# Performance work log

Hardware: AMD Instinct MI355X
Metric: run time of the kernel (lower is better)

Reference implementation:

```python
import jax, jax.numpy as jnp
import numpy as np

EPS = 1e-4
MAX_LAPLACE_VAR = 1000.0
MAX_DENSITY = 10000.0
BINS = 256

_LAP_KERNEL = jnp.array([[0., 1., 0.], [1., -4., 1.], [0., 1., 0.]], dtype=jnp.float32)[None, None]  # OIHW [1,1,3,3]


def setup_inputs() -> dict:
    key = jax.random.key(0)
    k1, k2 = jax.random.split(key)
    rgb_img = jax.random.uniform(k1, (32, 3, 512, 512), dtype=jnp.float32)
    depth_img = jax.random.normal(k2, (32, 1, 512, 512), dtype=jnp.float32)
    return {"rgb_img": rgb_img, "depth_img": depth_img}


def _rgb_confidence(rgb_img):
    B, C, H, W = rgb_img.shape
    gray = 0.299 * rgb_img[:, 0] + 0.587 * rgb_img[:, 1] + 0.114 * rgb_img[:, 2]  # [B,H,W]
    gray = gray[:, None]  # [B,1,H,W]
    lap = jax.lax.conv_general_dilated(
        gray, _LAP_KERNEL, window_strides=(1, 1), padding=[(1, 1), (1, 1)],
        dimension_numbers=("NCHW", "OIHW", "NCHW"))
    # torch.var default is unbiased (ddof=1)
    laplace_var = jnp.var(lap, axis=(1, 2, 3), ddof=1)

    # integer-valued pixels 0..255 land exactly in histc bins 0..255 (bins=256, min=0, max=255)
    vals = jnp.clip(gray * 255.0, 0.0, 255.0).astype(jnp.int32)  # [B,1,H,W]
    vals = vals.reshape(B, -1)  # [B, H*W]
    bidx = jnp.broadcast_to(jnp.arange(B)[:, None], vals.shape)
    hist = jnp.zeros((B, BINS), jnp.float32).at[bidx, vals].add(1.0)
    p = hist / jnp.sum(hist, axis=1, keepdims=True)
    entropy = -jnp.sum(p * jnp.log2(p + EPS), axis=1)

    clarity_score = laplace_var / (MAX_LAPLACE_VAR + EPS)
    uniformity_score = 1.0 / (entropy + EPS)
    return (0.5 * (clarity_score + uniformity_score))[:, None]  # [B,1]


def _depth_confidence(depth_img):
    C = depth_img.shape[1]
    depth_map = depth_img[:, 2] if C == 3 else depth_img[:, 0]  # [B,H,W]
    mask = (depth_map > 0).astype(jnp.float32)
    density = jnp.mean(mask, axis=(1, 2))

    # vectorized masked std (unbiased, ddof=1), matching torch.std over valid pixels
    n = jnp.sum(mask, axis=(1, 2))  # [B]
    mean = jnp.sum(depth_map * mask, axis=(1, 2)) / jnp.maximum(n, 1.0)
    sq = jnp.sum(mask * (depth_map - mean[:, None, None]) ** 2, axis=(1, 2))
    var = sq / jnp.maximum(n - 1.0, 1.0)
    std = jnp.sqrt(jnp.maximum(var, 0.0))
    noise_level = jnp.where(n > 0, std, 1.0)

    density_score = density / (MAX_DENSITY + EPS)
    noise_score = 1.0 / (noise_level + EPS)
    return (0.5 * (density_score + noise_score))[:, None]  # [B,1]


def reference(rgb_img, depth_img):
    rgb_conf = _rgb_confidence(rgb_img)
    depth_conf = _depth_confidence(depth_img)
    denom = rgb_conf + depth_conf + EPS
    w_r = rgb_conf / denom
    w_d = depth_conf / denom
    return (w_r, w_d)
```

## Files before the change

### kernel.cpp

```cpp
#include <hip/hip_runtime.h>

#define IMG_H 512
#define IMG_W 512
#define HW (IMG_H * IMG_W)
#define NB 32
#define ROWS 16
#define STRIPS (IMG_H / ROWS)

#define ACC_DOUBLES 160
#define WS_BYTES (ACC_DOUBLES * 8 + NB * 256 * 4)

__device__ inline void wave_reduce2(double& a, double& b) {
    for (int off = 32; off > 0; off >>= 1) {
        a += __shfl_down(a, off, 64);
        b += __shfl_down(b, off, 64);
    }
}

__global__ __launch_bounds__(256) void rgb_kernel(
    const float* __restrict__ rgb,
    double* __restrict__ lap_sum, double* __restrict__ lap_sq,
    unsigned int* __restrict__ hist)
{
    __shared__ float g[ROWS + 2][IMG_W];
    __shared__ unsigned int lh[256];
    __shared__ double r1s[4], r2s[4];

    const int t = threadIdx.x;
    const int b = blockIdx.y;
    const int row0 = blockIdx.x * ROWS;

    lh[t] = 0u;

    const float* rp = rgb + (size_t)b * 3 * HW;
    const float* gp = rp + HW;
    const float* bp = gp + HW;

    const int c0 = t * 2;
    for (int j = 0; j < ROWS + 2; ++j) {
        const int gr = row0 + j - 1;
        float gx = 0.f, gy = 0.f;
        if (gr >= 0 && gr < IMG_H) {
            const size_t o = (size_t)gr * IMG_W + c0;
            const float2 r2 = *(const float2*)(rp + o);
            const float2 g2 = *(const float2*)(gp + o);
            const float2 b2 = *(const float2*)(bp + o);
            gx = 0.299f * r2.x + 0.587f * g2.x + 0.114f * b2.x;
            gy = 0.299f * r2.y + 0.587f * g2.y + 0.114f * b2.y;
        }
        g[j][c0] = gx;
        g[j][c0 + 1] = gy;
    }
    __syncthreads();

    float s1 = 0.f, s2 = 0.f;
    for (int i = 0; i < ROWS * IMG_W / 256; ++i) {
        const int p = i * 256 + t;
        const int r = (p >> 9) + 1;
        const int c = p & (IMG_W - 1);
        const float center = g[r][c];
        float lap = g[r - 1][c] + g[r + 1][c] - 4.f * center;
        lap += (c > 0) ? g[r][c - 1] : 0.f;
        lap += (c < IMG_W - 1) ? g[r][c + 1] : 0.f;
        s1 += lap;
        s2 += lap * lap;
        const float v = fminf(fmaxf(center * 255.f, 0.f), 255.f);
        atomicAdd(&lh[(int)v], 1u);
    }

    double d1 = (double)s1, d2 = (double)s2;
    wave_reduce2(d1, d2);
    const int wid = t >> 6, lane = t & 63;
    if (lane == 0) { r1s[wid] = d1; r2s[wid] = d2; }
    __syncthreads();

    atomicAdd(&hist[b * 256 + t], lh[t]);
    if (t == 0) {
        atomicAdd(&lap_sum[b], r1s[0] + r1s[1] + r1s[2] + r1s[3]);
        atomicAdd(&lap_sq[b],  r2s[0] + r2s[1] + r2s[2] + r2s[3]);
    }
}

__global__ __launch_bounds__(256) void depth_kernel(
    const float* __restrict__ depth,
    double* __restrict__ dn, double* __restrict__ dsum, double* __restrict__ dsq)
{
    __shared__ double rns[4], rss[4], rqs[4];
    const int t = threadIdx.x;
    const int b = blockIdx.y;
    const size_t base = (size_t)b * HW + (size_t)blockIdx.x * (HW / 32);
    const float4* p4 = (const float4*)(depth + base);

    float n = 0.f, s = 0.f, q = 0.f;
    for (int i = 0; i < 8; ++i) {
        const float4 v = p4[i * 256 + t];
        if (v.x > 0.f) { n += 1.f; s += v.x; q += v.x * v.x; }
        if (v.y > 0.f) { n += 1.f; s += v.y; q += v.y * v.y; }
        if (v.z > 0.f) { n += 1.f; s += v.z; q += v.z * v.z; }
        if (v.w > 0.f) { n += 1.f; s += v.w; q += v.w * v.w; }
    }

    double dn_ = (double)n, ds_ = (double)s, dq_ = (double)q;
    for (int off = 32; off > 0; off >>= 1) {
        dn_ += __shfl_down(dn_, off, 64);
        ds_ += __shfl_down(ds_, off, 64);
        dq_ += __shfl_down(dq_, off, 64);
    }
    const int wid = t >> 6, lane = t & 63;
    if (lane == 0) { rns[wid] = dn_; rss[wid] = ds_; rqs[wid] = dq_; }
    __syncthreads();
    if (t == 0) {
        atomicAdd(&dn[b],   rns[0] + rns[1] + rns[2] + rns[3]);
        atomicAdd(&dsum[b], rss[0] + rss[1] + rss[2] + rss[3]);
        atomicAdd(&dsq[b],  rqs[0] + rqs[1] + rqs[2] + rqs[3]);
    }
}

__global__ void final_kernel(
    const double* __restrict__ acc,
    const unsigned int* __restrict__ hist,
    float* __restrict__ out)
{
    const int b = threadIdx.x;
    if (b >= NB) return;
    const double N = (double)HW;

    double e = 0.0;
    for (int k = 0; k < 256; ++k) {
        const float p = (float)hist[b * 256 + k] * (1.0f / (float)HW);
        e += (double)(p * log2f(p + 1e-4f));
    }
    const double entropy = -e;

    const double ls = acc[b], lq = acc[32 + b];
    const double lvar = (lq - ls * ls / N) / (N - 1.0);
    const double clarity = lvar / (1000.0 + 1e-4);
    const double uniformity = 1.0 / (entropy + 1e-4);
    const double rgb_conf = 0.5 * (clarity + uniformity);

    const double n = acc[64 + b], s = acc[96 + b], q = acc[128 + b];
    const double mean = s / fmax(n, 1.0);
    const double sq = q - 2.0 * mean * s + mean * mean * n;
    const double var = sq / fmax(n - 1.0, 1.0);
    const double stdd = sqrt(fmax(var, 0.0));
    const double noise = (n > 0.0) ? stdd : 1.0;
    const double density = n / N;
    const double depth_conf = 0.5 * (density / (10000.0 + 1e-4) + 1.0 / (noise + 1e-4));

    const double denom = rgb_conf + depth_conf + 1e-4;
    out[b]      = (float)(rgb_conf / denom);
    out[NB + b] = (float)(depth_conf / denom);
}

extern "C" void kernel_launch(void* const* d_in, const int* in_sizes, int n_in,
                              void* d_out, int out_size, void* d_ws, size_t ws_size,
                              hipStream_t stream) {
    const float* rgb   = (const float*)d_in[0];
    const float* depth = (const float*)d_in[1];
    float* out = (float*)d_out;

    double* acc = (double*)d_ws;
    unsigned int* hist = (unsigned int*)((char*)d_ws + ACC_DOUBLES * 8);

    hipMemsetAsync(d_ws, 0, WS_BYTES, stream);

    rgb_kernel<<<dim3(STRIPS, NB), 256, 0, stream>>>(rgb, acc, acc + 32, hist);
    depth_kernel<<<dim3(32, NB), 256, 0, stream>>>(depth, acc + 64, acc + 96, acc + 128);
    final_kernel<<<1, 64, 0, stream>>>(acc, hist, out);
}
```

Baseline: 202.2 us.

## Fuse RGB and depth reductions into one kernel and vectorize stencil loads

Merges the RGB Laplacian/histogram kernel and the depth statistics kernel into a single launch. Each block prefetches its depth slice into registers before loading the RGB strip, so the two streams' memory traffic overlaps. The RGB loads and Laplacian stencil now use float4 accesses, and the final entropy pass is spread over 256 threads instead of one per batch. Holding the depth prefetch in registers raises register pressure, and launch_bounds(256,4) may force spills.

After: 192.8 us. -4.7%, faster.

```diff
diff --git a/kernel.cpp b/kernel.cpp
--- a/kernel.cpp
+++ b/kernel.cpp
@@ -10,146 +10,149 @@
 #define ACC_DOUBLES 160
 #define WS_BYTES (ACC_DOUBLES * 8 + NB * 256 * 4)
 
-__device__ inline void wave_reduce2(double& a, double& b) {
+__global__ __launch_bounds__(256, 4) void fused_kernel(
+    const float* __restrict__ rgb, const float* __restrict__ depth,
+    double* __restrict__ acc, unsigned int* __restrict__ hist)
+{
+    __shared__ float g[ROWS + 2][IMG_W];
+    __shared__ unsigned int lh[256];
+    __shared__ double red[4][5];
+
+    const int t = threadIdx.x;
+    const int b = blockIdx.y;
+    const int s = blockIdx.x;
+    const int row0 = s * ROWS;
+
+    lh[t] = 0u;
+
+    const float4* dp = (const float4*)(depth + (size_t)b * HW + (size_t)s * (HW / STRIPS));
+    float4 dv[8];
+    #pragma unroll
+    for (int i = 0; i < 8; ++i) dv[i] = dp[i * 256 + t];
+
+    const float* rp = rgb + (size_t)b * 3 * HW;
+    const int half = t >> 7;
+    const int c4 = (t & 127) << 2;
+    #pragma unroll
+    for (int j = 0; j < 9; ++j) {
+        const int lr = 2 * j + half;
+        const int gr = row0 + lr - 1;
+        float4 gv = {0.f, 0.f, 0.f, 0.f};
+        if (gr >= 0 && gr < IMG_H) {
+            const size_t o = (size_t)gr * IMG_W + c4;
+            const float4 r4 = *(const float4*)(rp + o);
+            const float4 g4 = *(const float4*)(rp + HW + o);
+            const float4 b4 = *(const float4*)(rp + 2 * HW + o);
+            gv.x = 0.299f * r4.x + 0.587f * g4.x + 0.114f * b4.x;
+            gv.y = 0.299f * r4.y + 0.587f * g4.y + 0.114f * b4.y;
+            gv.z = 0.299f * r4.z + 0.587f * g4.z + 0.114f * b4.z;
+            gv.w = 0.299f * r4.w + 0.587f * g4.w + 0.114f * b4.w;
+        }
+        *(float4*)&g[lr][c4] = gv;
+    }
+
+    float dnf = 0.f, dsf = 0.f, dqf = 0.f;
+    #pragma unroll
+    for (int i = 0; i < 8; ++i) {
+        const float4 v = dv[i];
+        if (v.x > 0.f) { dnf += 1.f; dsf += v.x; dqf += v.x * v.x; }
+        if (v.y > 0.f) { dnf += 1.f; dsf += v.y; dqf += v.y * v.y; }
+        if (v.z > 0.f) { dnf += 1.f; dsf += v.z; dqf += v.z * v.z; }
+        if (v.w > 0.f) { dnf += 1.f; dsf += v.w; dqf += v.w * v.w; }
+    }
+
+    __syncthreads();
+
+    float s1 = 0.f, s2 = 0.f;
+    #pragma unroll
+    for (int i = 0; i < 8; ++i) {
+        const int gi = i * 256 + t;
+        const int r = (gi >> 7) + 1;
+        const int c = (gi & 127) << 2;
+        const float4 ce = *(const float4*)&g[r][c];
+        const float4 up = *(const float4*)&g[r - 1][c];
+        const float4 dn = *(const float4*)&g[r + 1][c];
+        const float lf = (c > 0) ? g[r][c - 1] : 0.f;
+        const float rt = (c < IMG_W - 4) ? g[r][c + 4] : 0.f;
+        float4 lap;
+        lap.x = up.x + dn.x + lf   + ce.y - 4.f * ce.x;
+        lap.y = up.y + dn.y + ce.x + ce.z - 4.f * ce.y;
+        lap.z = up.z + dn.z + ce.y + ce.w - 4.f * ce.z;
+        lap.w = up.w + dn.w + ce.z + rt   - 4.f * ce.w;
+        s1 += lap.x + lap.y + lap.z + lap.w;
+        s2 += lap.x * lap.x + lap.y * lap.y + lap.z * lap.z + lap.w * lap.w;
+        atomicAdd(&lh[(int)fminf(fmaxf(ce.x * 255.f, 0.f), 255.f)], 1u);
+        atomicAdd(&lh[(int)fminf(fmaxf(ce.y * 255.f, 0.f), 255.f)], 1u);
+        atomicAdd(&lh[(int)fminf(fmaxf(ce.z * 255.f, 0.f), 255.f)], 1u);
+        atomicAdd(&lh[(int)fminf(fmaxf(ce.w * 255.f, 0.f), 255.f)], 1u);
+    }
+
+    double z0 = (double)s1, z1 = (double)s2, z2 = (double)dnf, z3 = (double)dsf, z4 = (double)dqf;
     for (int off = 32; off > 0; off >>= 1) {
-        a += __shfl_down(a, off, 64);
-        b += __shfl_down(b, off, 64);
+        z0 += __shfl_down(z0, off, 64);
+        z1 += __shfl_down(z1, off, 64);
+        z2 += __shfl_down(z2, off, 64);
+        z3 += __shfl_down(z3, off, 64);
+        z4 += __shfl_down(z4, off, 64);
+    }
+    const int wid = t >> 6, lane = t & 63;
+    if (lane == 0) {
+        red[wid][0] = z0; red[wid][1] = z1; red[wid][2] = z2;
+        red[wid][3] = z3; red[wid][4] = z4;
+    }
+    __syncthreads();
+
+    atomicAdd(&hist[b * 256 + t], lh[t]);
+    if (t < 5) {
+        const double v = red[0][t] + red[1][t] + red[2][t] + red[3][t];
+        atomicAdd(&acc[t * 32 + b], v);
     }
 }
 
-__global__ __launch_bounds__(256) void rgb_kernel(
-    const float* __restrict__ rgb,
-    double* __restrict__ lap_sum, double* __restrict__ lap_sq,
-    unsigned int* __restrict__ hist)
-{
-    __shared__ float g[ROWS + 2][IMG_W];
-    __shared__ unsigned int lh[256];
-    __shared__ double r1s[4], r2s[4];
-
-    const int t = threadIdx.x;
-    const int b = blockIdx.y;
-    const int row0 = blockIdx.x * ROWS;
-
-    lh[t] = 0u;
-
-    const float* rp = rgb + (size_t)b * 3 * HW;
-    const float* gp = rp + HW;
-    const float* bp = gp + HW;
-
-    const int c0 = t * 2;
-    for (int j = 0; j < ROWS + 2; ++j) {
-        const int gr = row0 + j - 1;
-        float gx = 0.f, gy = 0.f;
-        if (gr >= 0 && gr < IMG_H) {
-            const size_t o = (size_t)gr * IMG_W + c0;
-            const float2 r2 = *(const float2*)(rp + o);
-            const float2 g2 = *(const float2*)(gp + o);
-            const float2 b2 = *(const float2*)(bp + o);
-            gx = 0.299f * r2.x + 0.587f * g2.x + 0.114f * b2.x;
-            gy = 0.299f * r2.y + 0.587f * g2.y + 0.114f * b2.y;
-        }
-        g[j][c0] = gx;
-        g[j][c0 + 1] = gy;
-    }
-    __syncthreads();
-
-    float s1 = 0.f, s2 = 0.f;
-    for (int i = 0; i < ROWS * IMG_W / 256; ++i) {
-        const int p = i * 256 + t;
-        const int r = (p >> 9) + 1;
-        const int c = p & (IMG_W - 1);
-        const float center = g[r][c];
-        float lap = g[r - 1][c] + g[r + 1][c] - 4.f * center;
-        lap += (c > 0) ? g[r][c - 1] : 0.f;
-        lap += (c < IMG_W - 1) ? g[r][c + 1] : 0.f;
-        s1 += lap;
-        s2 += lap * lap;
-        const float v = fminf(fmaxf(center * 255.f, 0.f), 255.f);
-        atomicAdd(&lh[(int)v], 1u);
-    }
-
-    double d1 = (double)s1, d2 = (double)s2;
-    wave_reduce2(d1, d2);
-    const int wid = t >> 6, lane = t & 63;
-    if (lane == 0) { r1s[wid] = d1; r2s[wid] = d2; }
-    __syncthreads();
-
-    atomicAdd(&hist[b * 256 + t], lh[t]);
-    if (t == 0) {
-        atomicAdd(&lap_sum[b], r1s[0] + r1s[1] + r1s[2] + r1s[3]);
-        atomicAdd(&lap_sq[b],  r2s[0] + r2s[1] + r2s[2] + r2s[3]);
-    }
-}
-
-__global__ __launch_bounds__(256) void depth_kernel(
-    const float* __restrict__ depth,
-    double* __restrict__ dn, double* __restrict__ dsum, double* __restrict__ dsq)
-{
-    __shared__ double rns[4], rss[4], rqs[4];
-    const int t = threadIdx.x;
-    const int b = blockIdx.y;
-    const size_t base = (size_t)b * HW + (size_t)blockIdx.x * (HW / 32);
-    const float4* p4 = (const float4*)(depth + base);
-
-    float n = 0.f, s = 0.f, q = 0.f;
-    for (int i = 0; i < 8; ++i) {
-        const float4 v = p4[i * 256 + t];
-        if (v.x > 0.f) { n += 1.f; s += v.x; q += v.x * v.x; }
-        if (v.y > 0.f) { n += 1.f; s += v.y; q += v.y * v.y; }
-        if (v.z > 0.f) { n += 1.f; s += v.z; q += v.z * v.z; }
-        if (v.w > 0.f) { n += 1.f; s += v.w; q += v.w * v.w; }
-    }
-
-    double dn_ = (double)n, ds_ = (double)s, dq_ = (double)q;
-    for (int off = 32; off > 0; off >>= 1) {
-        dn_ += __shfl_down(dn_, off, 64);
-        ds_ += __shfl_down(ds_, off, 64);
-        dq_ += __shfl_down(dq_, off, 64);
-    }
-    const int wid = t >> 6, lane = t & 63;
-    if (lane == 0) { rns[wid] = dn_; rss[wid] = ds_; rqs[wid] = dq_; }
-    __syncthreads();
-    if (t == 0) {
-        atomicAdd(&dn[b],   rns[0] + rns[1] + rns[2] + rns[3]);
-        atomicAdd(&dsum[b], rss[0] + rss[1] + rss[2] + rss[3]);
-        atomicAdd(&dsq[b],  rqs[0] + rqs[1] + rqs[2] + rqs[3]);
-    }
-}
-
-__global__ void final_kernel(
+__global__ __launch_bounds__(256) void final_kernel(
     const double* __restrict__ acc,
     const unsigned int* __restrict__ hist,
     float* __restrict__ out)
 {
-    const int b = threadIdx.x;
-    if (b >= NB) return;
-    const double N = (double)HW;
+    __shared__ float part[256];
+    const int t = threadIdx.x;
+    const int b = t >> 3;
+    const int sl = t & 7;
+    float e = 0.f;
+    #pragma unroll
+    for (int i = 0; i < 32; ++i) {
+        const float p = (float)hist[b * 256 + sl * 32 + i] * (1.0f / (float)HW);
+        e += p * log2f(p + 1e-4f);
+    }
+    part[t] = e;
+    __syncthreads();
 
-    double e = 0.0;
-    for (int k = 0; k < 256; ++k) {
-        const float p = (float)hist[b * 256 + k] * (1.0f / (float)HW);
-        e += (double)(p * log2f(p + 1e-4f));
+    if (t < NB) {
+        float es = 0.f;
+        #pragma unroll
+        for (int i = 0; i < 8; ++i) es += part[t * 8 + i];
+        const double entropy = -(double)es;
+        const double N = (double)HW;
+
+        const double ls = acc[t], lq = acc[32 + t];
+        const double lvar = (lq - ls * ls / N) / (N - 1.0);
+        const double clarity = lvar / (1000.0 + 1e-4);
+        const double uniformity = 1.0 / (entropy + 1e-4);
+        const double rgb_conf = 0.5 * (clarity + uniformity);
+
+        const double n = acc[64 + t], sdep = acc[96 + t], q = acc[128 + t];
+        const double mean = sdep / fmax(n, 1.0);
+        const double sq = q - 2.0 * mean * sdep + mean * mean * n;
+        const double var = sq / fmax(n - 1.0, 1.0);
+        const double stdd = sqrt(fmax(var, 0.0));
+        const double noise = (n > 0.0) ? stdd : 1.0;
+        const double density = n / N;
+        const double depth_conf = 0.5 * (density / (10000.0 + 1e-4) + 1.0 / (noise + 1e-4));
+
+        const double denom = rgb_conf + depth_conf + 1e-4;
+        out[t]      = (float)(rgb_conf / denom);
+        out[NB + t] = (float)(depth_conf / denom);
     }
-    const double entropy = -e;
-
-    const double ls = acc[b], lq = acc[32 + b];
-    const double lvar = (lq - ls * ls / N) / (N - 1.0);
-    const double clarity = lvar / (1000.0 + 1e-4);
-    const double uniformity = 1.0 / (entropy + 1e-4);
-    const double rgb_conf = 0.5 * (clarity + uniformity);
-
-    const double n = acc[64 + b], s = acc[96 + b], q = acc[128 + b];
-    const double mean = s / fmax(n, 1.0);
-    const double sq = q - 2.0 * mean * s + mean * mean * n;
-    const double var = sq / fmax(n - 1.0, 1.0);
-    const double stdd = sqrt(fmax(var, 0.0));
-    const double noise = (n > 0.0) ? stdd : 1.0;
-    const double density = n / N;
-    const double depth_conf = 0.5 * (density / (10000.0 + 1e-4) + 1.0 / (noise + 1e-4));
-
-    const double denom = rgb_conf + depth_conf + 1e-4;
-    out[b]      = (float)(rgb_conf / denom);
-    out[NB + b] = (float)(depth_conf / denom);
 }
 
 extern "C" void kernel_launch(void* const* d_in, const int* in_sizes, int n_in,
@@ -164,7 +167,6 @@
 
     hipMemsetAsync(d_ws, 0, WS_BYTES, stream);
 
-    rgb_kernel<<<dim3(STRIPS, NB), 256, 0, stream>>>(rgb, acc, acc + 32, hist);
-    depth_kernel<<<dim3(32, NB), 256, 0, stream>>>(depth, acc + 64, acc + 96, acc + 128);
-    final_kernel<<<1, 64, 0, stream>>>(acc, hist, out);
+    fused_kernel<<<dim3(STRIPS, NB), 256, 0, stream>>>(rgb, depth, acc, hist);
+    final_kernel<<<1, 256, 0, stream>>>(acc, hist, out);
 }
```
